# Kernel optimization log

Measured on AMD Instinct MI355X. Metric: run time of the kernel, lower is better.

The kernel has to match this reference:

```python
import jax, jax.numpy as jnp
import numpy as np

B, S, D = 2, 2048, 768
H, STRIDE = 12, 8
HD = D // H  # 64


def setup_inputs() -> dict:
    key = jax.random.key(0)
    k0, k1, k2 = jax.random.split(key, 3)
    x = jax.random.normal(k0, (B, S, D), dtype=jnp.float32)
    qkv_w = jax.random.normal(k1, (3 * D, D), dtype=jnp.float32) * 0.02
    qkv_b = jnp.zeros((3 * D,), dtype=jnp.float32)
    out_w = jax.random.normal(k2, (D, D), dtype=jnp.float32) * 0.02
    out_b = jnp.zeros((D,), dtype=jnp.float32)
    return {"x": x, "qkv_w": qkv_w, "qkv_b": qkv_b, "out_w": out_w, "out_b": out_b}


def _stride_mask(S, stride, causal):
    i = jnp.arange(S)[:, None]
    j = jnp.arange(S)[None, :]
    strided = (j % stride == 0)
    if causal:
        strided = strided & (j <= i)
    # diagonal always attended; previous token attended for i > 0
    return strided | (j == i) | (j == i - 1)


def reference(x, qkv_w, qkv_b, out_w, out_b):
    Bx, Sx, Dx = x.shape
    qkv = x @ qkv_w.T + qkv_b                      # [B,S,3D]
    qkv = qkv.reshape(Bx, Sx, 3, H, HD)
    q, k, v = jnp.transpose(qkv, (2, 0, 3, 1, 4))  # each [B,H,S,HD]
    scale = HD ** -0.5
    attn = jnp.einsum('bhid,bhjd->bhij', q, k) * scale  # [B,H,S,S]
    mask = _stride_mask(Sx, STRIDE, True)          # [S,S] bool
    attn = jnp.where(mask[None, None], attn, -jnp.inf)
    a = jax.nn.softmax(attn, axis=-1)
    # every row has at least the diagonal unmasked, so no NaN rows;
    # nan_to_num kept for exact parity with the torch module
    a = jnp.nan_to_num(a, nan=0.0)
    out = jnp.einsum('bhij,bhjd->bhid', a, v)      # [B,H,S,HD]
    out = jnp.transpose(out, (0, 2, 1, 3)).reshape(Bx, Sx, Dx)
    return out @ out_w.T + out_b
```

## Files before the change

### kernel.cpp

```cpp
#include <hip/hip_runtime.h>
#include <hip/hip_bf16.h>
#include <stdint.h>

#define H_   12
#define S_   2048
#define D_   768
#define HD_  64
#define MS_  256

typedef __bf16 bf16_8 __attribute__((ext_vector_type(8)));
typedef float  f32_4  __attribute__((ext_vector_type(4)));

typedef __attribute__((address_space(1))) void* gas_ptr;
typedef __attribute__((address_space(3))) void* las_ptr;

__device__ __forceinline__ void g2l16(const void* g, void* l) {
  __builtin_amdgcn_global_load_lds((gas_ptr)g, (las_ptr)l, 16, 0, 0);
}

__device__ __forceinline__ f32_4 mfma16(bf16_8 a, bf16_8 b, f32_4 c) {
  return __builtin_amdgcn_mfma_f32_16x16x32_bf16(a, b, c, 0, 0, 0);
}

__device__ __forceinline__ bf16_8 ld8(const __hip_bfloat16* p) {
  return *reinterpret_cast<const bf16_8*>(p);
}

__global__ __launch_bounds__(256) void cvt3_f32_bf16(
    const float* __restrict__ a, const float* __restrict__ b,
    const float* __restrict__ c, __hip_bfloat16* __restrict__ out,
    int na4, int nb4) {
  const int t = blockIdx.x * 256 + threadIdx.x;
  float4 f;
  if (t < na4)            f = reinterpret_cast<const float4*>(a)[t];
  else if (t < na4 + nb4) f = reinterpret_cast<const float4*>(b)[t - na4];
  else                    f = reinterpret_cast<const float4*>(c)[t - na4 - nb4];
  union { __hip_bfloat16 h[4]; ushort4 u; } p;
  p.h[0] = __float2bfloat16(f.x);
  p.h[1] = __float2bfloat16(f.y);
  p.h[2] = __float2bfloat16(f.z);
  p.h[3] = __float2bfloat16(f.w);
  reinterpret_cast<ushort4*>(out)[t] = p.u;
}

template <int MODE, int BN>
__global__ __launch_bounds__(256, 4) void gemm_bt(
    const __hip_bfloat16* __restrict__ A, const __hip_bfloat16* __restrict__ B,
    const float* __restrict__ bias,
    __hip_bfloat16* __restrict__ O0, __hip_bfloat16* __restrict__ O1,
    __hip_bfloat16* __restrict__ O2, __hip_bfloat16* __restrict__ O3,
    __hip_bfloat16* __restrict__ O4, float* __restrict__ OF,
    int M, int N, int K) {
  constexpr int NTJ = BN / 32;
  constexpr int HB  = BN * 32;
  __shared__ __bf16 sA[2 * 64 * 32];
  __shared__ __bf16 sB[2 * BN * 32];
  const int tid  = threadIdx.x;
  const int lane = tid & 63;
  const int wv   = tid >> 6;

  const int nwg  = gridDim.x * gridDim.y;
  const int hw   = blockIdx.y * gridDim.x + blockIdx.x;
  const int swz  = (hw & 7) * (nwg >> 3) + (hw >> 3);
  const int bx   = swz % gridDim.x;
  const int by   = swz / gridDim.x;

  const int m0 = by * 64;
  const int n0 = bx * BN;
  const int wr = (wv >> 1) * 32;
  const int wc = (wv & 1) * (BN / 2);

  f32_4 acc[2][NTJ] = {};

  const __hip_bfloat16* aS = A + (size_t)(m0 + (tid >> 2)) * K + ((tid & 3) << 3);
  const __hip_bfloat16* bS = B + (size_t)(n0 + (tid >> 2)) * K + ((tid & 3) << 3);
  const size_t half = (size_t)64 * K;
  __bf16* dA = &sA[tid * 8];
  __bf16* dB = &sB[tid * 8];

  const int fr = lane & 15;
  const int kq = (lane >> 4) << 3;

  for (int k0 = 0; k0 < K; k0 += 64) {
    g2l16(aS,      dA);
    g2l16(aS + 32, dA + 2048);
    g2l16(bS,      dB);
    if constexpr (BN == 128) {
      g2l16(bS + half,      dB + 2048);
      g2l16(bS + 32,        dB + 4096);
      g2l16(bS + half + 32, dB + 4096 + 2048);
    } else {
      g2l16(bS + 32, dB + 2048);
    }
    aS += 64;
    bS += 64;
    __syncthreads();

#pragma unroll
    for (int kk = 0; kk < 2; ++kk) {
      bf16_8 af[2], bfm[NTJ];
#pragma unroll
      for (int t = 0; t < 2; ++t)
        af[t] = *reinterpret_cast<const bf16_8*>(
            &sA[kk * 2048 + (wr + t * 16 + fr) * 32 + kq]);
#pragma unroll
      for (int t = 0; t < NTJ; ++t)
        bfm[t] = *reinterpret_cast<const bf16_8*>(
            &sB[kk * HB + (wc + t * 16 + fr) * 32 + kq]);
#pragma unroll
      for (int ti = 0; ti < 2; ++ti)
#pragma unroll
        for (int tj = 0; tj < NTJ; ++tj)
          acc[ti][tj] = mfma16(af[ti], bfm[tj], acc[ti][tj]);
    }
    __syncthreads();
  }

  const int crow = (lane >> 4) << 2;
  const int ccol = lane & 15;
#pragma unroll
  for (int ti = 0; ti < 2; ++ti) {
    const int gmb = m0 + wr + ti * 16 + crow;
#pragma unroll
    for (int tj = 0; tj < NTJ; ++tj) {
      const int gn = n0 + wc + tj * 16 + ccol;
      const float bv = bias[gn];
      if (MODE == 0) {
        const int t   = gn / D_;
        const int rem = gn - t * D_;
        const int hh = rem >> 6, dd = rem & 63;
        __hip_bfloat16* dst = (t == 0) ? O0 : (t == 1) ? O1 : O2;
#pragma unroll
        for (int r = 0; r < 4; ++r) {
          const int gm = gmb + r;
          const int bb = gm >> 11, ss = gm & (S_ - 1);
          const __hip_bfloat16 hv = __float2bfloat16(acc[ti][tj][r] + bv);
          dst[(((size_t)(bb * H_ + hh) << 11) + ss) * HD_ + dd] = hv;
          if (r == 0 && (gmb & 7) == 0) {
            if (t == 1)
              O4[(((size_t)(bb * H_ + hh)) * MS_ + (ss >> 3)) * HD_ + dd] = hv;
            else if (t == 2)
              O3[((size_t)(bb * H_ + hh) * HD_ + dd) * MS_ + (ss >> 3)] = hv;
          }
        }
      } else {
#pragma unroll
        for (int r = 0; r < 4; ++r)
          OF[(size_t)(gmb + r) * D_ + gn] = acc[ti][tj][r] + bv;
      }
    }
  }
}

__global__ __launch_bounds__(256) void attn_mfma(
    const __hip_bfloat16* __restrict__ Q, const __hip_bfloat16* __restrict__ Kb,
    const __hip_bfloat16* __restrict__ Ks, const __hip_bfloat16* __restrict__ Vr,
    const __hip_bfloat16* __restrict__ VsT, __hip_bfloat16* __restrict__ ctx) {
  __shared__ __bf16 pt[4][16 * 40];
  __shared__ float ox[3][64][20];
  const int lane = threadIdx.x & 63;
  const int part = threadIdx.x >> 6;
  const int task = blockIdx.x;
  const int bh   = task >> 7;
  const int i0   = (task & 127) << 4;
  const int lr   = lane & 15;
  const int quad = lane >> 4;
  const float SC = 0.125f * 1.44269504088896340736f;

  const __hip_bfloat16* Kh  = Kb  + ((size_t)bh << 11) * HD_;
  const __hip_bfloat16* Ksh = Ks  + (size_t)bh * MS_ * HD_;
  const __hip_bfloat16* Vrh = Vr  + ((size_t)bh << 11) * HD_;
  const __hip_bfloat16* Vsh = VsT + (size_t)bh * HD_ * MS_;
  __bf16* ptw = pt[part];

  const int jbase = (i0 >= 8) ? (i0 - 8) : 0;

  bf16_8 vfb[4], kb_[2][2];
  if (part == 3) {
    const __bf16* Vrb = reinterpret_cast<const __bf16*>(Vrh);
#pragma unroll
    for (int ct = 0; ct < 4; ++ct)
#pragma unroll
      for (int e = 0; e < 8; ++e) {
        const int j  = jbase + quad * 8 + e;
        const int jr = (j < S_) ? j : (S_ - 1);
        vfb[ct][e] = Vrb[(size_t)jr * HD_ + ct * 16 + lr];
      }
#pragma unroll
    for (int t = 0; t < 2; ++t) {
      const int j  = jbase + t * 16 + lr;
      const int jr = (j < S_) ? j : (S_ - 1);
      const __hip_bfloat16* kp = Kh + (size_t)jr * HD_ + quad * 8;
      kb_[t][0] = ld8(kp);
      kb_[t][1] = ld8(kp + 32);
    }
  }

  const __hip_bfloat16* qp = Q + (((size_t)bh << 11) + i0 + lr) * HD_ + quad * 8;
  const bf16_8 qf0 = ld8(qp);
  const bf16_8 qf1 = ld8(qp + 32);

  const __bf16 one = (__bf16)1.0f;
  const bf16_8 onesf = {one, one, one, one, one, one, one, one};

  f32_4 Lacc = {}, oacc[4];
#pragma unroll
  for (int ct = 0; ct < 4; ++ct) oacc[ct] = f32_4{0.f, 0.f, 0.f, 0.f};

  const int mmax = (i0 + 15) >> 3;
  const int nstr = (mmax >> 5) + 1;

  auto load_str = [&](int c, bf16_8 (&kf)[2][2], bf16_8 (&vf)[4]) {
    const int mb = c << 5;
#pragma unroll
    for (int t = 0; t < 2; ++t) {
      const __hip_bfloat16* kp = Ksh + (size_t)(mb + t * 16 + lr) * HD_ + quad * 8;
      kf[t][0] = ld8(kp);
      kf[t][1] = ld8(kp + 32);
    }
#pragma unroll
    for (int ct = 0; ct < 4; ++ct)
      vf[ct] = ld8(Vsh + (size_t)(ct * 16 + lr) * MS_ + mb + quad * 8);
  };

  auto softmax_pv = [&](f32_4& s0, f32_4& s1, const bf16_8 (&vf)[4]) {
#pragma unroll
    for (int r = 0; r < 4; ++r) {
      const int row = quad * 4 + r;
      ptw[row * 40 + lr]      = (__bf16)__float2bfloat16(s0[r]);
      ptw[row * 40 + 16 + lr] = (__bf16)__float2bfloat16(s1[r]);
    }
    const bf16_8 pf = *reinterpret_cast<const bf16_8*>(&ptw[lr * 40 + quad * 8]);
#pragma unroll
    for (int ct = 0; ct < 4; ++ct) oacc[ct] = mfma16(pf, vf[ct], oacc[ct]);
    Lacc = mfma16(pf, onesf, Lacc);
  };

  bf16_8 kf[2][2], vf[4], kf2[2][2], vf2[4];
  if (part < nstr) load_str(part, kf, vf);
  for (int c = part; c < nstr; c += 4) {
    const bool more = (c + 4 < nstr);
    if (more) load_str(c + 4, kf2, vf2);
    const int mb = c << 5;

    f32_4 s0 = {}, s1 = {};
    s0 = mfma16(qf0, kf[0][0], s0);
    s0 = mfma16(qf1, kf[0][1], s0);
    s1 = mfma16(qf0, kf[1][0], s1);
    s1 = mfma16(qf1, kf[1][1], s1);

#pragma unroll
    for (int r = 0; r < 4; ++r) {
      const int i = i0 + quad * 4 + r;
      const bool v0 = ((mb + lr) << 3) <= i;
      const bool v1 = ((mb + 16 + lr) << 3) <= i;
      s0[r] = v0 ? exp2f(fminf(s0[r] * SC, 63.f)) : 0.f;
      s1[r] = v1 ? exp2f(fminf(s1[r] * SC, 63.f)) : 0.f;
    }
    softmax_pv(s0, s1, vf);

    if (more) {
#pragma unroll
      for (int t = 0; t < 2; ++t) { kf[t][0] = kf2[t][0]; kf[t][1] = kf2[t][1]; }
#pragma unroll
      for (int ct = 0; ct < 4; ++ct) vf[ct] = vf2[ct];
    }
  }

  if (part == 3) {
    f32_4 s0 = {}, s1 = {};
    s0 = mfma16(qf0, kb_[0][0], s0);
    s0 = mfma16(qf1, kb_[0][1], s0);
    s1 = mfma16(qf0, kb_[1][0], s1);
    s1 = mfma16(qf1, kb_[1][1], s1);

#pragma unroll
    for (int r = 0; r < 4; ++r) {
      const int i = i0 + quad * 4 + r;
      const int j0 = jbase + lr, j1 = jbase + 16 + lr;
      const bool v0 = (j0 == i || j0 == i - 1) && (j0 & 7);
      const bool v1 = (j1 == i || j1 == i - 1) && (j1 & 7);
      s0[r] = v0 ? exp2f(fminf(s0[r] * SC, 63.f)) : 0.f;
      s1[r] = v1 ? exp2f(fminf(s1[r] * SC, 63.f)) : 0.f;
    }
    softmax_pv(s0, s1, vfb);
  }

  if (part) {
#pragma unroll
    for (int ct = 0; ct < 4; ++ct)
#pragma unroll
      for (int r = 0; r < 4; ++r) ox[part - 1][lane][ct * 4 + r] = oacc[ct][r];
#pragma unroll
    for (int r = 0; r < 4; ++r) ox[part - 1][lane][16 + r] = Lacc[r];
  }
  __syncthreads();

  if (!part) {
#pragma unroll
    for (int p = 0; p < 3; ++p) {
#pragma unroll
      for (int ct = 0; ct < 4; ++ct)
#pragma unroll
        for (int r = 0; r < 4; ++r) oacc[ct][r] += ox[p][lane][ct * 4 + r];
#pragma unroll
      for (int r = 0; r < 4; ++r) Lacc[r] += ox[p][lane][16 + r];
    }

    const int b = bh / H_;
    const int h = bh - b * H_;
    f32_4 inv;
#pragma unroll
    for (int r = 0; r < 4; ++r) inv[r] = 1.f / Lacc[r];
#pragma unroll
    for (int r = 0; r < 4; ++r) {
      const int i = i0 + quad * 4 + r;
      __hip_bfloat16* cp = ctx + ((size_t)(b * S_ + i)) * D_ + h * HD_ + lr;
#pragma unroll
      for (int ct = 0; ct < 4; ++ct)
        cp[ct * 16] = __float2bfloat16(oacc[ct][r] * inv[r]);
    }
  }
}

extern "C" void kernel_launch(void* const* d_in, const int* in_sizes, int n_in,
                              void* d_out, int out_size, void* d_ws, size_t ws_size,
                              hipStream_t stream) {
  const float* x    = (const float*)d_in[0];
  const float* qkvw = (const float*)d_in[1];
  const float* qkvb = (const float*)d_in[2];
  const float* outw = (const float*)d_in[3];
  const float* outb = (const float*)d_in[4];
  float* out = (float*)d_out;

  const size_t NX  = (size_t)2 * S_ * D_;
  const size_t NW1 = (size_t)3 * D_ * D_;
  const size_t NW2 = (size_t)D_ * D_;
  const size_t NVS = (size_t)2 * H_ * HD_ * MS_;

  __hip_bfloat16* xb  = (__hip_bfloat16*)d_ws;
  __hip_bfloat16* w1b = xb + NX;
  __hip_bfloat16* w2b = w1b + NW1;
  __hip_bfloat16* q   = w2b + NW2;
  __hip_bfloat16* k   = q + NX;
  __hip_bfloat16* vr  = k + NX;
  __hip_bfloat16* vst = vr + NX;
  __hip_bfloat16* ks  = vst + NVS;
  __hip_bfloat16* ctx = ks + NVS;

  const int na4 = (int)(NX / 4), nb4 = (int)(NW1 / 4), nc4 = (int)(NW2 / 4);
  cvt3_f32_bf16<<<dim3((na4 + nb4 + nc4) / 256), 256, 0, stream>>>(
      x, qkvw, outw, xb, na4, nb4);

  gemm_bt<0, 128><<<dim3(2304 / 128, 4096 / 64), 256, 0, stream>>>(
      xb, w1b, qkvb, q, k, vr, vst, ks, nullptr, 4096, 2304, 768);

  attn_mfma<<<dim3(2 * H_ * S_ / 16), 256, 0, stream>>>(
      q, k, ks, vr, vst, ctx);

  gemm_bt<1, 64><<<dim3(768 / 64, 4096 / 64), 256, 0, stream>>>(
      ctx, w2b, outb, nullptr, nullptr, nullptr, nullptr, nullptr,
      out, 4096, 768, 768);
}
```

Baseline: 139.8 us.

## Assign one query tile per wavefront instead of splitting strided keys across waves

The attention kernel used to have four wavefronts cooperate on one 16-row query tile, splitting the strided key chunks among them and reducing partial outputs through shared memory with a block barrier. Now each wavefront owns its own query tile and walks all strided chunks itself, so the LDS reduction and __syncthreads go away, and the grid shrinks by a factor of four. Query tiles are also issued in reverse order so the longest causal rows start first, which helps load balancing. The trade-off is less parallelism per tile and longer serial loops for late rows, plus imbalance among the four waves sharing a block.

Result: slower. 143.9 us (+2.9%).

```diff
diff --git a/kernel.cpp b/kernel.cpp
--- a/kernel.cpp
+++ b/kernel.cpp
@@ -157,12 +157,12 @@
     const __hip_bfloat16* __restrict__ Ks, const __hip_bfloat16* __restrict__ Vr,
     const __hip_bfloat16* __restrict__ VsT, __hip_bfloat16* __restrict__ ctx) {
   __shared__ __bf16 pt[4][16 * 40];
-  __shared__ float ox[3][64][20];
   const int lane = threadIdx.x & 63;
-  const int part = threadIdx.x >> 6;
-  const int task = blockIdx.x;
+  const int wv   = threadIdx.x >> 6;
+  const int task = blockIdx.x * 4 + wv;
   const int bh   = task >> 7;
-  const int i0   = (task & 127) << 4;
+  const int qt   = 127 - (task & 127);
+  const int i0   = qt << 4;
   const int lr   = lane & 15;
   const int quad = lane >> 4;
   const float SC = 0.125f * 1.44269504088896340736f;
@@ -171,12 +171,12 @@
   const __hip_bfloat16* Ksh = Ks  + (size_t)bh * MS_ * HD_;
   const __hip_bfloat16* Vrh = Vr  + ((size_t)bh << 11) * HD_;
   const __hip_bfloat16* Vsh = VsT + (size_t)bh * HD_ * MS_;
-  __bf16* ptw = pt[part];
+  __bf16* ptw = pt[wv];
 
   const int jbase = (i0 >= 8) ? (i0 - 8) : 0;
 
   bf16_8 vfb[4], kb_[2][2];
-  if (part == 3) {
+  {
     const __bf16* Vrb = reinterpret_cast<const __bf16*>(Vrh);
 #pragma unroll
     for (int ct = 0; ct < 4; ++ct)
@@ -237,10 +237,10 @@
   };
 
   bf16_8 kf[2][2], vf[4], kf2[2][2], vf2[4];
-  if (part < nstr) load_str(part, kf, vf);
-  for (int c = part; c < nstr; c += 4) {
-    const bool more = (c + 4 < nstr);
-    if (more) load_str(c + 4, kf2, vf2);
+  load_str(0, kf, vf);
+  for (int c = 0; c < nstr; ++c) {
+    const bool more = (c + 1 < nstr);
+    if (more) load_str(c + 1, kf2, vf2);
     const int mb = c << 5;
 
     f32_4 s0 = {}, s1 = {};
@@ -267,7 +267,7 @@
     }
   }
 
-  if (part == 3) {
+  {
     f32_4 s0 = {}, s1 = {};
     s0 = mfma16(qf0, kb_[0][0], s0);
     s0 = mfma16(qf1, kb_[0][1], s0);
@@ -286,27 +286,7 @@
     softmax_pv(s0, s1, vfb);
   }
 
-  if (part) {
-#pragma unroll
-    for (int ct = 0; ct < 4; ++ct)
-#pragma unroll
-      for (int r = 0; r < 4; ++r) ox[part - 1][lane][ct * 4 + r] = oacc[ct][r];
-#pragma unroll
-    for (int r = 0; r < 4; ++r) ox[part - 1][lane][16 + r] = Lacc[r];
-  }
-  __syncthreads();
-
-  if (!part) {
-#pragma unroll
-    for (int p = 0; p < 3; ++p) {
-#pragma unroll
-      for (int ct = 0; ct < 4; ++ct)
-#pragma unroll
-        for (int r = 0; r < 4; ++r) oacc[ct][r] += ox[p][lane][ct * 4 + r];
-#pragma unroll
-      for (int r = 0; r < 4; ++r) Lacc[r] += ox[p][lane][16 + r];
-    }
-
+  {
     const int b = bh / H_;
     const int h = bh - b * H_;
     f32_4 inv;
@@ -355,7 +335,7 @@
   gemm_bt<0, 128><<<dim3(2304 / 128, 4096 / 64), 256, 0, stream>>>(
       xb, w1b, qkvb, q, k, vr, vst, ks, nullptr, 4096, 2304, 768);
 
-  attn_mfma<<<dim3(2 * H_ * S_ / 16), 256, 0, stream>>>(
+  attn_mfma<<<dim3(2 * H_ * S_ / 16 / 4), 256, 0, stream>>>(
       q, k, ks, vr, vst, ctx);
 
   gemm_bt<1, 64><<<dim3(768 / 64, 4096 / 64), 256, 0, stream>>>(
```
